# Performance work log

Hardware: AMD Instinct MI355X
Metric: run time of the kernel (lower is better)

Reference implementation:

```python
import jax, jax.numpy as jnp
import numpy as np

B, H, W, DM = 4, 64, 64, 96
DS, DC, K = 16, 3, 4
DI = DM            # expand = 1.0
DTR = 6            # ceil(96/16)


def setup_inputs() -> dict:
    key = jax.random.key(0)
    ks = jax.random.split(key, 12)
    s = 0.02
    # dt bias init exactly as MS2D.dt_init: dt ~ exp(U*(log(max)-log(min))+log(min)); inv softplus
    dt = jnp.exp(jax.random.uniform(ks[5], (K, DI)) * (np.log(0.1) - np.log(0.001)) + np.log(0.001))
    dt = jnp.clip(dt, 1e-4, None)
    inv_dt = dt + jnp.log(-jnp.expm1(-dt))
    A_logs = jnp.log(jnp.broadcast_to(jnp.arange(1, DS + 1, dtype=jnp.float32), (K, DI, DS)))
    return {
        "x": jax.random.normal(ks[0], (B, H, W, DM), jnp.float32),
        "in_proj_w": jax.random.normal(ks[1], (2 * DI, DM), jnp.float32) * s,
        "conv_w": jax.random.normal(ks[2], (DI, 1, DC, DC), jnp.float32) * s,
        "conv_b": jnp.zeros((DI,), jnp.float32),
        "x_proj_weight": jax.random.normal(ks[3], (K, DTR + 2 * DS, DI), jnp.float32) * s,
        "dt_projs_weight": jax.random.uniform(ks[4], (K, DI, DTR), minval=-1.0, maxval=1.0) * (DTR ** -0.5),
        "dt_projs_bias": inv_dt,
        "A_logs": A_logs,
        "Ds": jnp.ones((K, DI), jnp.float32),
        "out_norm_w": jnp.ones((DI,), jnp.float32),
        "out_norm_b": jnp.zeros((DI,), jnp.float32),
        "out_proj_w": jax.random.normal(ks[6], (DM, DI), jnp.float32) * s,
    }


def _ms2d(x, in_proj_w, conv_w, conv_b, x_proj_weight, dt_projs_weight,
          dt_projs_bias, A_logs, Ds, out_norm_w, out_norm_b, out_proj_w):
    Bb, Hh, Ww, _ = x.shape
    L = Hh * Ww
    # in_proj -> (x, z) gating split
    xz = x @ in_proj_w.T                      # (B,H,W,2*DI)
    xc, z = jnp.split(xz, 2, axis=-1)
    xc = jnp.transpose(xc, (0, 3, 1, 2))      # (B,DI,H,W)
    xc = jax.lax.conv_general_dilated(
        xc, conv_w, (1, 1), 'SAME', feature_group_count=xc.shape[1],
        dimension_numbers=('NCHW', 'OIHW', 'NCHW')) + conv_b[None, :, None, None]
    xc = jax.nn.silu(xc)
    d = xc.shape[1]
    # 4-directional scan sequences: hw, wh, and their reverses
    x_hw = xc.reshape(Bb, d, L)
    x_wh = jnp.transpose(xc, (0, 1, 3, 2)).reshape(Bb, d, L)
    x2 = jnp.stack([x_hw, x_wh], axis=1)          # (B,2,d,L)
    xs = jnp.concatenate([x2, jnp.flip(x2, axis=-1)], axis=1)  # (B,4,d,L)
    x_dbl = jnp.einsum('bkdl,kcd->bkcl', xs, x_proj_weight)
    dtr = dt_projs_weight.shape[2]
    n = A_logs.shape[2]
    dts, Bs, Cs = jnp.split(x_dbl, [dtr, dtr + n], axis=2)     # (B,4,r,L),(B,4,N,L),(B,4,N,L)
    dts = jnp.einsum('bkrl,kdr->bkdl', dts, dt_projs_weight)
    delta = jax.nn.softplus(dts + dt_projs_bias[None, :, :, None])  # (B,4,d,L)
    A = -jnp.exp(A_logs)                                        # (4,d,N)
    # time-major for scan
    u_t = jnp.moveaxis(xs, -1, 0)       # (L,B,4,d)
    dl_t = jnp.moveaxis(delta, -1, 0)
    B_t = jnp.moveaxis(Bs, -1, 0)       # (L,B,4,N)
    C_t = jnp.moveaxis(Cs, -1, 0)

    def step(h, inp):                   # h: (B,4,d,N)
        u, dl, b, c = inp
        dA = jnp.exp(dl[..., None] * A)
        h = h * dA + (dl * u)[..., None] * b[:, :, None, :]
        y = jnp.einsum('bkdn,bkn->bkd', h, c)
        return h, y

    h0 = jnp.zeros((Bb, 4, d, n), xs.dtype)
    _, ys = jax.lax.scan(step, h0, (u_t, dl_t, B_t, C_t))
    ys = jnp.moveaxis(ys, 0, -1)        # (B,4,d,L)
    ys = ys + Ds[None, :, :, None] * xs  # skip D*u
    inv_y = jnp.flip(ys[:, 2:4], axis=-1)

    def wh2hw(t):  # undo the (W,H) raster order
        return jnp.transpose(t.reshape(Bb, d, Ww, Hh), (0, 1, 3, 2)).reshape(Bb, d, L)

    y = ys[:, 0] + inv_y[:, 0] + wh2hw(ys[:, 1]) + wh2hw(inv_y[:, 1])
    y = jnp.transpose(y, (0, 2, 1)).reshape(Bb, Hh, Ww, d)
    mu = y.mean(-1, keepdims=True)
    var = y.var(-1, keepdims=True)
    y = (y - mu) / jnp.sqrt(var + 1e-5) * out_norm_w + out_norm_b
    y = y * jax.nn.silu(z)
    return y @ out_proj_w.T


def reference(x, in_proj_w, conv_w, conv_b, x_proj_weight, dt_projs_weight,
              dt_projs_bias, A_logs, Ds, out_norm_w, out_norm_b, out_proj_w):
    return _ms2d(x, in_proj_w, conv_w, conv_b, x_proj_weight, dt_projs_weight,
                 dt_projs_bias, A_logs, Ds, out_norm_w, out_norm_b, out_proj_w)
```

## Files before the change

### kernel.cpp

```cpp
#include <hip/hip_runtime.h>
#include <math.h>


#define LQ 4096
#define NCH 128
#define LCH 32

__device__ __forceinline__ float sigmoid_f(float x){ return 1.0f/(1.0f + __expf(-x)); }
__device__ __forceinline__ float silu_f(float x){ return x * sigmoid_f(x); }
__device__ __forceinline__ float softplus_f(float x){ return (x > 20.0f) ? x : __logf(1.0f + __expf(x)); }

__device__ __forceinline__ int pos_of(int k, int i){
  switch(k & 3){
    case 0: return i;
    case 1: return ((i & 63) << 6) | (i >> 6);
    case 2: return LQ - 1 - i;
    default: { int j = LQ - 1 - i; return ((j & 63) << 6) | (j >> 6); }
  }
}

__device__ __forceinline__ void pow8(float r, int nh, float* e){
  e[0]=r; e[1]=r*r; e[2]=e[1]*r; e[3]=e[1]*e[1];
  e[4]=e[3]*r; e[5]=e[3]*e[1]; e[6]=e[3]*e[2]; e[7]=e[3]*e[3];
  float m = nh ? e[7] : 1.0f;
  #pragma unroll
  for (int j=0;j<8;j++) e[j] *= m;
}

__global__ __launch_bounds__(64) void k_prep(const float* __restrict__ Alogs,
                                             float* __restrict__ An_tab,
                                             float* __restrict__ fflag){
  const int t = blockIdx.x*64 + threadIdx.x;
  if (t >= 384) return;
  bool fast = true;
  #pragma unroll
  for (int n=0;n<16;n++){
    float An = -__expf(Alogs[t*16+n]);
    An_tab[t*16+n] = An;
    fast = fast && (fabsf(An + (float)(n+1)) < 1e-3f*(float)(n+1));
  }
  fflag[t] = fast ? 1.0f : 0.0f;
}

__global__ __launch_bounds__(256) void k_inproj(const float* __restrict__ x,
                                                const float* __restrict__ wproj,
                                                float* __restrict__ xc,
                                                float* __restrict__ zb){
  __shared__ float a_s[64*97];
  __shared__ float w_s[96*97];
  const int t = threadIdx.x;
  const int row0 = (blockIdx.x >> 1) * 64;
  const int ch = blockIdx.x & 1;
  for (int e = t*4; e < 64*96; e += 1024){
    float4 v = *(const float4*)(x + (size_t)row0*96 + e);
    int r = e/96, c = e%96;
    float* p = a_s + r*97 + c;
    p[0]=v.x; p[1]=v.y; p[2]=v.z; p[3]=v.w;
  }
  for (int e = t*4; e < 96*96; e += 1024){
    float4 v = *(const float4*)(wproj + (size_t)ch*96*96 + e);
    int r = e/96, c = e%96;
    float* p = w_s + r*97 + c;
    p[0]=v.x; p[1]=v.y; p[2]=v.z; p[3]=v.w;
  }
  __syncthreads();
  const int tr = t >> 5, tc = t & 31;
  float acc[8][3];
  #pragma unroll
  for (int i=0;i<8;i++){
    #pragma unroll
    for (int j=0;j<3;j++) acc[i][j]=0.f;
  }
  for (int kk=0; kk<96; kk++){
    float a[8], b[3];
    #pragma unroll
    for (int i=0;i<8;i++) a[i] = a_s[(tr*8+i)*97+kk];
    #pragma unroll
    for (int j=0;j<3;j++) b[j] = w_s[(tc*3+j)*97+kk];
    #pragma unroll
    for (int i=0;i<8;i++){
      #pragma unroll
      for (int j=0;j<3;j++) acc[i][j] += a[i]*b[j];
    }
  }
  float* dst = ch ? zb : xc;
  #pragma unroll
  for (int i=0;i<8;i++){
    int row = row0 + tr*8 + i;
    #pragma unroll
    for (int j=0;j<3;j++) dst[(size_t)row*96 + tc*3 + j] = acc[i][j];
  }
}

__global__ __launch_bounds__(256) void k_conv(const float* __restrict__ xc,
                                              const float* __restrict__ cw,
                                              const float* __restrict__ cb,
                                              float* __restrict__ u){
  int e = blockIdx.x*256 + threadIdx.x;
  int d0 = (e % 24) * 4;
  int p = e / 24;
  int w = p & 63, h = (p >> 6) & 63, b = p >> 12;
  float cwv[4][9];
  #pragma unroll
  for (int q=0;q<4;q++){
    #pragma unroll
    for (int tp=0;tp<9;tp++) cwv[q][tp] = cw[(d0+q)*9+tp];
  }
  float4 acc = make_float4(cb[d0], cb[d0+1], cb[d0+2], cb[d0+3]);
  #pragma unroll
  for (int kh=0; kh<3; kh++){
    int hh = h + kh - 1;
    if (hh < 0 || hh > 63) continue;
    #pragma unroll
    for (int kw=0; kw<3; kw++){
      int ww = w + kw - 1;
      if (ww < 0 || ww > 63) continue;
      float4 v = *(const float4*)(xc + ((size_t)((b<<12) + (hh<<6) + ww))*96 + d0);
      int tp = kh*3+kw;
      acc.x += v.x*cwv[0][tp]; acc.y += v.y*cwv[1][tp];
      acc.z += v.z*cwv[2][tp]; acc.w += v.w*cwv[3][tp];
    }
  }
  float4 o = make_float4(silu_f(acc.x), silu_f(acc.y), silu_f(acc.z), silu_f(acc.w));
  *(float4*)(u + (size_t)p*96 + d0) = o;
}

__global__ __launch_bounds__(128) void k_proj(const float* __restrict__ u,
                                              const float* __restrict__ xpw,
                                              float* __restrict__ dts,
                                              float* __restrict__ Bsb,
                                              float* __restrict__ Csb){
  __shared__ float u_s[64*97];
  __shared__ float w_s[40*97];
  const int t = threadIdx.x;
  const int blk = blockIdx.x;
  const int pt = blk & 63, k = (blk >> 6) & 3, b = blk >> 8;
  const int bk = b*4 + k;
  const int i0 = pt * 64;
  for (int e = t*4; e < 64*96; e += 512){
    int row = e/96, c = e%96;
    int p = pos_of(k, i0 + row);
    float4 v = *(const float4*)(u + ((size_t)((b<<12) + p))*96 + c);
    float* dst = u_s + row*97 + c;
    dst[0]=v.x; dst[1]=v.y; dst[2]=v.z; dst[3]=v.w;
  }
  for (int e = t*4; e < 40*96; e += 512){
    int r = e/96, c = e%96;
    float4 v = (r < 38) ? *(const float4*)(xpw + (k*38+r)*96 + c)
                        : make_float4(0,0,0,0);
    float* p = w_s + r*97 + c;
    p[0]=v.x; p[1]=v.y; p[2]=v.z; p[3]=v.w;
  }
  __syncthreads();
  const int posg = t & 15, cg = t >> 4;
  float acc[4][5];
  #pragma unroll
  for (int i=0;i<4;i++){
    #pragma unroll
    for (int j=0;j<5;j++) acc[i][j]=0.f;
  }
  for (int dd=0; dd<96; dd++){
    float uu[4], wv[5];
    #pragma unroll
    for (int i=0;i<4;i++) uu[i] = u_s[(posg*4+i)*97+dd];
    #pragma unroll
    for (int j=0;j<5;j++) wv[j] = w_s[(cg*5+j)*97+dd];
    #pragma unroll
    for (int i=0;i<4;i++){
      #pragma unroll
      for (int j=0;j<5;j++) acc[i][j] += uu[i]*wv[j];
    }
  }
  #pragma unroll
  for (int i=0;i<4;i++){
    int ii = i0 + posg*4 + i;
    int base = (bk<<12) + ii;
    #pragma unroll
    for (int j=0;j<5;j++){
      int c = cg*5 + j;
      float v = acc[i][j];
      if (c < 6)       dts[(size_t)base*6 + c] = v;
      else if (c < 22) Bsb[(size_t)base*16 + (c-6)] = v;
      else if (c < 38) Csb[(size_t)base*16 + (c-22)] = v;
    }
  }
}

__global__ __launch_bounds__(384, 2) void k_scanA2(const float* __restrict__ u,
                                                const float* __restrict__ dts,
                                                const float* __restrict__ Bsb,
                                                const float* __restrict__ Csb,
                                                const float* __restrict__ dtw_g,
                                                const float* __restrict__ dtb_g,
                                                const float* __restrict__ An_tab,
                                                const float* __restrict__ fflag,
                                                float* __restrict__ S,
                                                float* __restrict__ sumd,
                                                float* __restrict__ ys,
                                                float* __restrict__ cum_g){
  const int t = threadIdx.x;
  const int c2 = t / 192;
  const int lane = t & 63;
  const int wv3 = (t % 192) >> 6;
  const int nh = (lane >> 5) & 1;
  const int d = wv3*32 + (lane & 31);
  const int blk = blockIdx.x;
  const int bk = blk >> 6;
  const int k = bk & 3, b = bk >> 2;
  const int chunk = ((blk & 63) << 1) | c2;
  const int ibase = chunk * LCH;
  const int kd = k*96 + d;
  int wfast = __all(fflag[kd] > 0.5f ? 1 : 0);
  float An[8];
  #pragma unroll
  for (int j=0;j<8;j++) An[j] = An_tab[kd*16 + nh*8 + j];
  float dtw[6];
  #pragma unroll
  for (int r=0;r<6;r++) dtw[r] = dtw_g[kd*6+r];
  const float bias = dtb_g[kd];
  const int pb = pos_of(k, ibase);
  const int pstep = pos_of(k, ibase+1) - pb;
  const float* uptr = u + ((size_t)((b<<12)+pb))*96 + d;
  const long ustep = (long)pstep*96;
  const float2* dtp = (const float2*)(dts + ((size_t)((bk<<12)+ibase))*6);
  const float4* Bp = (const float4*)(Bsb + ((size_t)((bk<<12)+ibase))*16) + nh*2;
  const float4* Cp = (const float4*)(Csb + ((size_t)((bk<<12)+ibase))*16) + nh*2;
  float* yp = ys + ((size_t)((bk<<12)+ibase))*96 + d;
  float* cp = cum_g + ((size_t)((bk<<12)+ibase))*96 + d;
  float h[8];
  #pragma unroll
  for (int n=0;n<8;n++) h[n]=0.f;
  float cum = 0.f;
  float u_n = uptr[0];
  float2 q0n = dtp[0], q1n = dtp[1], q2n = dtp[2];
  float4 B0n = Bp[0], B1n = Bp[1];
  float4 C0n = Cp[0], C1n = Cp[1];
  if (wfast){
    #pragma unroll 4
    for (int il=0; il<LCH; il++){
      float u_c = u_n;
      float2 q0=q0n, q1=q1n, q2=q2n;
      float4 B0=B0n, B1=B1n, C0=C0n, C1=C1n;
      const int nx = (il+1 < LCH) ? il+1 : il;
      u_n = uptr[(long)nx*ustep];
      q0n = dtp[nx*3+0]; q1n = dtp[nx*3+1]; q2n = dtp[nx*3+2];
      B0n = Bp[nx*4+0]; B1n = Bp[nx*4+1];
      C0n = Cp[nx*4+0]; C1n = Cp[nx*4+1];
      float accd = bias + dtw[0]*q0.x + dtw[1]*q0.y + dtw[2]*q1.x
                        + dtw[3]*q1.y + dtw[4]*q2.x + dtw[5]*q2.y;
      float t1 = __expf(accd);
      float r = 1.0f/(1.0f+t1);
      float delta = (accd > 20.f) ? accd : __logf(1.0f + t1);
      cum += delta;
      float du = delta * u_c;
      float Bv[8] = {B0.x,B0.y,B0.z,B0.w, B1.x,B1.y,B1.z,B1.w};
      float Cv[8] = {C0.x,C0.y,C0.z,C0.w, C1.x,C1.y,C1.z,C1.w};
      float e[8];
      pow8(r, nh, e);
      float y8 = 0.f;
      #pragma unroll
      for (int n=0;n<8;n++){
        h[n] = h[n]*e[n] + du*Bv[n];
        y8 += h[n]*Cv[n];
      }
      float y = y8 + __shfl_xor(y8, 32, 64);
      if (nh == 0){ yp[(size_t)il*96] = y; cp[(size_t)il*96] = cum; }
    }
  } else {
    #pragma unroll 2
    for (int il=0; il<LCH; il++){
      float u_c = u_n;
      float2 q0=q0n, q1=q1n, q2=q2n;
      float4 B0=B0n, B1=B1n, C0=C0n, C1=C1n;
      const int nx = (il+1 < LCH) ? il+1 : il;
      u_n = uptr[(long)nx*ustep];
      q0n = dtp[nx*3+0]; q1n = dtp[nx*3+1]; q2n = dtp[nx*3+2];
      B0n = Bp[nx*4+0]; B1n = Bp[nx*4+1];
      C0n = Cp[nx*4+0]; C1n = Cp[nx*4+1];
      float accd = bias + dtw[0]*q0.x + dtw[1]*q0.y + dtw[2]*q1.x
                        + dtw[3]*q1.y + dtw[4]*q2.x + dtw[5]*q2.y;
      float delta = softplus_f(accd);
      cum += delta;
      float du = delta * u_c;
      float Bv[8] = {B0.x,B0.y,B0.z,B0.w, B1.x,B1.y,B1.z,B1.w};
      float Cv[8] = {C0.x,C0.y,C0.z,C0.w, C1.x,C1.y,C1.z,C1.w};
      float e[8];
      #pragma unroll
      for (int n=0;n<8;n++) e[n] = __expf(delta*An[n]);
      float y8 = 0.f;
      #pragma unroll
      for (int n=0;n<8;n++){
        h[n] = h[n]*e[n] + du*Bv[n];
        y8 += h[n]*Cv[n];
      }
      float y = y8 + __shfl_xor(y8, 32, 64);
      if (nh == 0){ yp[(size_t)il*96] = y; cp[(size_t)il*96] = cum; }
    }
  }
  const int sb = (bk*NCH + chunk)*96 + d;
  float4* Sp = (float4*)(S + (size_t)sb*16 + nh*8);
  Sp[0] = make_float4(h[0],h[1],h[2],h[3]);
  Sp[1] = make_float4(h[4],h[5],h[6],h[7]);
  if (nh == 0) sumd[sb] = cum;
}

__global__ __launch_bounds__(384) void k_scanA_fb(const float* __restrict__ u,
                                                  const float* __restrict__ dts,
                                                  const float* __restrict__ Bsb,
                                                  const float* __restrict__ dtw_g,
                                                  const float* __restrict__ dtb_g,
                                                  const float* __restrict__ Alogs,
                                                  float* __restrict__ S,
                                                  float* __restrict__ sumd){
  const int t = threadIdx.x;
  const int c2 = t / 192;
  const int lane = t & 63;
  const int wv3 = (t % 192) >> 6;
  const int nh = (lane >> 5) & 1;
  const int d = wv3*32 + (lane & 31);
  const int blk = blockIdx.x;
  const int bk = blk >> 6;
  const int k = bk & 3, b = bk >> 2;
  const int chunk = ((blk & 63) << 1) | c2;
  const int ibase = chunk * LCH;
  float An[8];
  bool fast = true;
  #pragma unroll
  for (int j=0;j<8;j++){
    int n = nh*8 + j;
    An[j] = -__expf(Alogs[(k*96+d)*16+n]);
    fast = fast && (fabsf(An[j] + (float)(n+1)) < 1e-3f*(float)(n+1));
  }
  int wfast = __all(fast ? 1 : 0);
  float dtw[6];
  #pragma unroll
  for (int r=0;r<6;r++) dtw[r] = dtw_g[(k*96+d)*6+r];
  const float bias = dtb_g[k*96+d];
  int pb = pos_of(k, ibase);
  int pstep = pos_of(k, ibase+1) - pb;
  const float* uptr = u + ((size_t)((b<<12)+pb))*96 + d;
  const long ustep = (long)pstep*96;
  const float2* dtp = (const float2*)(dts + ((size_t)((bk<<12)+ibase))*6);
  const float4* Bp = (const float4*)(Bsb + ((size_t)((bk<<12)+ibase))*16) + nh*2;
  float h[8];
  #pragma unroll
  for (int n=0;n<8;n++) h[n]=0.f;
  float sdelta = 0.f;
  #pragma unroll 4
  for (int il=0; il<LCH; il++){
    float uv = *uptr;
    float2 q0 = dtp[0], q1 = dtp[1], q2 = dtp[2];
    float accd = bias + dtw[0]*q0.x + dtw[1]*q0.y + dtw[2]*q1.x
                      + dtw[3]*q1.y + dtw[4]*q2.x + dtw[5]*q2.y;
    float t1 = __expf(accd);
    float r = 1.0f / (1.0f + t1);
    float delta = (accd > 20.f) ? accd : __logf(1.0f + t1);
    sdelta += delta;
    float du = delta * uv;
    float4 b0 = Bp[0], b1 = Bp[1];
    float Bv[8] = {b0.x,b0.y,b0.z,b0.w, b1.x,b1.y,b1.z,b1.w};
    float e[8];
    if (wfast){ pow8(r, nh, e); }
    else {
      #pragma unroll
      for (int n=0;n<8;n++) e[n] = __expf(delta*An[n]);
    }
    #pragma unroll
    for (int n=0;n<8;n++) h[n] = h[n]*e[n] + du*Bv[n];
    uptr += ustep; dtp += 3; Bp += 4;
  }
  const int sb = (bk*NCH + chunk)*96 + d;
  float4* Sp = (float4*)(S + (size_t)sb*16 + nh*8);
  Sp[0] = make_float4(h[0],h[1],h[2],h[3]);
  Sp[1] = make_float4(h[4],h[5],h[6],h[7]);
  if (nh == 0) sumd[sb] = sdelta;
}

__global__ __launch_bounds__(128) void k_scanB2(float* __restrict__ S,
                                                const float* __restrict__ sumd,
                                                const float* __restrict__ Alogs,
                                                const float* __restrict__ An_tab,
                                                const float* __restrict__ fflag){
  __shared__ float As[128*17];
  __shared__ float Bs[128*17];
  const int c = threadIdx.x;
  const int blk = blockIdx.x;
  const int d = blk % 96;
  const int bk = blk / 96;
  const int k = bk & 3;
  const int sb = (bk*NCH + c)*96 + d;
  float a[16], bvals[16];
  {
    const float4* Sp = (const float4*)(S + (size_t)sb*16);
    float4 s0=Sp[0], s1=Sp[1], s2=Sp[2], s3=Sp[3];
    bvals[0]=s0.x;bvals[1]=s0.y;bvals[2]=s0.z;bvals[3]=s0.w;
    bvals[4]=s1.x;bvals[5]=s1.y;bvals[6]=s1.z;bvals[7]=s1.w;
    bvals[8]=s2.x;bvals[9]=s2.y;bvals[10]=s2.z;bvals[11]=s2.w;
    bvals[12]=s3.x;bvals[13]=s3.y;bvals[14]=s3.z;bvals[15]=s3.w;
  }
  const float sd = sumd[sb];
  bool fast;
  float An[16];
  if (An_tab){
    fast = fflag[k*96+d] > 0.5f;
    if (!fast){
      #pragma unroll
      for (int n=0;n<16;n++) An[n] = An_tab[(k*96+d)*16+n];
    }
  } else {
    fast = true;
    #pragma unroll
    for (int n=0;n<16;n++){
      An[n] = -__expf(Alogs[(k*96+d)*16+n]);
      fast = fast && (fabsf(An[n] + (float)(n+1)) < 1e-3f*(float)(n+1));
    }
  }
  if (fast){
    float q = __expf(-sd);
    float p = q;
    #pragma unroll
    for (int n=0;n<16;n++){ a[n] = p; p *= q; }
  } else {
    #pragma unroll
    for (int n=0;n<16;n++) a[n] = __expf(An[n]*sd);
  }
  #pragma unroll
  for (int n=0;n<16;n++){ As[c*17+n] = a[n]; Bs[c*17+n] = bvals[n]; }
  for (int dist=1; dist<128; dist<<=1){
    __syncthreads();
    float aL[16], bL[16];
    if (c >= dist){
      #pragma unroll
      for (int n=0;n<16;n++){ aL[n] = As[(c-dist)*17+n]; bL[n] = Bs[(c-dist)*17+n]; }
    }
    __syncthreads();
    if (c >= dist){
      #pragma unroll
      for (int n=0;n<16;n++){
        bvals[n] = bL[n]*a[n] + bvals[n];
        a[n] = aL[n]*a[n];
        As[c*17+n] = a[n]; Bs[c*17+n] = bvals[n];
      }
    }
  }
  __syncthreads();
  float h0[16];
  #pragma unroll
  for (int n=0;n<16;n++) h0[n] = (c == 0) ? 0.f : Bs[(c-1)*17+n];
  float4* Sp = (float4*)(S + (size_t)sb*16);
  Sp[0] = make_float4(h0[0],h0[1],h0[2],h0[3]);
  Sp[1] = make_float4(h0[4],h0[5],h0[6],h0[7]);
  Sp[2] = make_float4(h0[8],h0[9],h0[10],h0[11]);
  Sp[3] = make_float4(h0[12],h0[13],h0[14],h0[15]);
}

__global__ __launch_bounds__(256) void k_scanY(const float* __restrict__ cum_g,
                                               const float* __restrict__ Csb,
                                               const float* __restrict__ An_tab,
                                               const float* __restrict__ fflag,
                                               const float* __restrict__ h0buf,
                                               float* __restrict__ ys){
  __shared__ float h0_s[32*17];
  __shared__ float An_s[32*17];
  __shared__ float ff_s[32];
  const int t = threadIdx.x;
  const int blk = blockIdx.x;
  const int dslice = blk % 3;
  const int tmp = blk / 3;
  const int chunk = tmp & 127;
  const int bk = tmp >> 7;
  const int k = bk & 3;
  const int dbase = dslice * 32;
  {
    const float* h0src = h0buf + ((size_t)((bk*NCH + chunk)*96 + dbase))*16;
    const float* Ansrc = An_tab + (size_t)(k*96 + dbase)*16;
    for (int e = t; e < 512; e += 256){
      int dl = e >> 4, n = e & 15;
      h0_s[dl*17+n] = h0src[e];
      An_s[dl*17+n] = Ansrc[e];
    }
    if (t < 32) ff_s[t] = fflag[k*96 + dbase + t];
  }
  __syncthreads();
  const int il = t >> 3;
  const int dq = t & 7;
  const int d0 = dbase + dq*4;
  const int i = chunk*LCH + il;
  const size_t rowb = (size_t)((bk<<12) + i);
  float4 cd = *(const float4*)(cum_g + rowb*96 + d0);
  float4 yl = *(const float4*)(ys + rowb*96 + d0);
  float Cv[16];
  {
    const float4* Cp = (const float4*)(Csb + rowb*16);
    float4 c0=Cp[0], c1=Cp[1], c2=Cp[2], c3=Cp[3];
    Cv[0]=c0.x;Cv[1]=c0.y;Cv[2]=c0.z;Cv[3]=c0.w;
    Cv[4]=c1.x;Cv[5]=c1.y;Cv[6]=c1.z;Cv[7]=c1.w;
    Cv[8]=c2.x;Cv[9]=c2.y;Cv[10]=c2.z;Cv[11]=c2.w;
    Cv[12]=c3.x;Cv[13]=c3.y;Cv[14]=c3.z;Cv[15]=c3.w;
  }
  float yout[4] = {yl.x, yl.y, yl.z, yl.w};
  float cdv[4] = {cd.x, cd.y, cd.z, cd.w};
  #pragma unroll
  for (int dd=0; dd<4; dd++){
    const int dl = dq*4 + dd;
    float acc = 0.f;
    if (ff_s[dl] > 0.5f){
      float q = __expf(-cdv[dd]);
      float p = q;
      #pragma unroll
      for (int n=0;n<16;n++){ acc += Cv[n]*h0_s[dl*17+n]*p; p *= q; }
    } else {
      #pragma unroll
      for (int n=0;n<16;n++) acc += Cv[n]*h0_s[dl*17+n]*__expf(An_s[dl*17+n]*cdv[dd]);
    }
    yout[dd] += acc;
  }
  *(float4*)(ys + rowb*96 + d0) = make_float4(yout[0], yout[1], yout[2], yout[3]);
}

__global__ __launch_bounds__(384) void k_scanC_fb(const float* __restrict__ u,
                                                  const float* __restrict__ dts,
                                                  const float* __restrict__ Bsb,
                                                  const float* __restrict__ Csb,
                                                  const float* __restrict__ dtw_g,
                                                  const float* __restrict__ dtb_g,
                                                  const float* __restrict__ Alogs,
                                                  const float* __restrict__ h0buf,
                                                  float* __restrict__ ys){
  const int t = threadIdx.x;
  const int c2 = t / 192;
  const int lane = t & 63;
  const int wv3 = (t % 192) >> 6;
  const int nh = (lane >> 5) & 1;
  const int d = wv3*32 + (lane & 31);
  const int blk = blockIdx.x;
  const int bk = blk >> 6;
  const int k = bk & 3, b = bk >> 2;
  const int chunk = ((blk & 63) << 1) | c2;
  const int ibase = chunk * LCH;
  float An[8];
  bool fast = true;
  #pragma unroll
  for (int j=0;j<8;j++){
    int n = nh*8 + j;
    An[j] = -__expf(Alogs[(k*96+d)*16+n]);
    fast = fast && (fabsf(An[j] + (float)(n+1)) < 1e-3f*(float)(n+1));
  }
  int wfast = __all(fast ? 1 : 0);
  float dtw[6];
  #pragma unroll
  for (int r=0;r<6;r++) dtw[r] = dtw_g[(k*96+d)*6+r];
  const float bias = dtb_g[k*96+d];
  int pb = pos_of(k, ibase);
  int pstep = pos_of(k, ibase+1) - pb;
  const float* uptr = u + ((size_t)((b<<12)+pb))*96 + d;
  const long ustep = (long)pstep*96;
  const float2* dtp = (const float2*)(dts + ((size_t)((bk<<12)+ibase))*6);
  const float4* Bp = (const float4*)(Bsb + ((size_t)((bk<<12)+ibase))*16) + nh*2;
  const float4* Cp = (const float4*)(Csb + ((size_t)((bk<<12)+ibase))*16) + nh*2;
  float* yp = ys + ((size_t)((bk<<12)+ibase))*96 + d;
  float h[8];
  const int sb = (bk*NCH + chunk)*96 + d;
  const float4* Hp = (const float4*)(h0buf + (size_t)sb*16 + nh*8);
  {
    float4 h0=Hp[0], h1=Hp[1];
    h[0]=h0.x;h[1]=h0.y;h[2]=h0.z;h[3]=h0.w;
    h[4]=h1.x;h[5]=h1.y;h[6]=h1.z;h[7]=h1.w;
  }
  #pragma unroll 4
  for (int il=0; il<LCH; il++){
    float uv = *uptr;
    float2 q0 = dtp[0], q1 = dtp[1], q2 = dtp[2];
    float accd = bias + dtw[0]*q0.x + dtw[1]*q0.y + dtw[2]*q1.x
                      + dtw[3]*q1.y + dtw[4]*q2.x + dtw[5]*q2.y;
    float t1 = __expf(accd);
    float r = 1.0f / (1.0f + t1);
    float delta = (accd > 20.f) ? accd : __logf(1.0f + t1);
    float du = delta * uv;
    float4 b0 = Bp[0], b1 = Bp[1];
    float4 c0 = Cp[0], c1 = Cp[1];
    float Bv[8] = {b0.x,b0.y,b0.z,b0.w, b1.x,b1.y,b1.z,b1.w};
    float Cv[8] = {c0.x,c0.y,c0.z,c0.w, c1.x,c1.y,c1.z,c1.w};
    float e[8];
    if (wfast){ pow8(r, nh, e); }
    else {
      #pragma unroll
      for (int n=0;n<8;n++) e[n] = __expf(delta*An[n]);
    }
    float y8 = 0.f;
    #pragma unroll
    for (int n=0;n<8;n++){
      h[n] = h[n]*e[n] + du*Bv[n];
      y8 += h[n]*Cv[n];
    }
    float y = y8 + __shfl_xor(y8, 32, 64);
    if (nh == 0) yp[(size_t)il*96] = y;
    uptr += ustep; dtp += 3; Bp += 4; Cp += 4;
  }
}

__global__ __launch_bounds__(256) void k_out(const float* __restrict__ ys,
                                             const float* __restrict__ ubuf,
                                             const float* __restrict__ Dsg,
                                             const float* __restrict__ zbuf,
                                             const float* __restrict__ nw,
                                             const float* __restrict__ nb,
                                             const float* __restrict__ wout,
                                             float* __restrict__ out){
  __shared__ float w_s[96*97];
  __shared__ float g_s[32*97];
  const int t = threadIdx.x;
  const int b = blockIdx.x >> 7;
  const int pt = blockIdx.x & 127;
  const int p0 = pt * 32;
  for (int e=t*4; e<96*96; e+=1024){
    float4 v = *(const float4*)(wout+e);
    int r=e/96, c=e%96;
    float* p = w_s + r*97 + c;
    p[0]=v.x; p[1]=v.y; p[2]=v.z; p[3]=v.w;
  }
  const int pos = t >> 3, lane8 = t & 7, d0 = lane8*12;
  const int p = p0 + pos;
  const int tp = ((p & 63) << 6) | (p >> 6);
  int idx[4];
  idx[0] = p; idx[1] = tp; idx[2] = LQ-1-p; idx[3] = LQ-1-tp;
  float yv[12];
  float s1=0.f, s2=0.f;
  #pragma unroll
  for (int i=0;i<12;i+=4){
    float4 a = make_float4(0,0,0,0);
    #pragma unroll
    for (int kk=0;kk<4;kk++){
      float4 v = *(const float4*)(ys + ((size_t)(((b*4+kk)<<12) + idx[kk]))*96 + d0 + i);
      a.x+=v.x; a.y+=v.y; a.z+=v.z; a.w+=v.w;
    }
    float4 uv = *(const float4*)(ubuf + ((size_t)((b<<12)+p))*96 + d0 + i);
    #pragma unroll
    for (int q=0;q<4;q++){
      int dd = d0+i+q;
      float sD = Dsg[dd] + Dsg[96+dd] + Dsg[192+dd] + Dsg[288+dd];
      float uq = (q==0)?uv.x:(q==1)?uv.y:(q==2)?uv.z:uv.w;
      float* aq = (q==0)?&a.x:(q==1)?&a.y:(q==2)?&a.z:&a.w;
      *aq += sD * uq;
    }
    yv[i]=a.x; yv[i+1]=a.y; yv[i+2]=a.z; yv[i+3]=a.w;
    s1 += a.x+a.y+a.z+a.w;
    s2 += a.x*a.x + a.y*a.y + a.z*a.z + a.w*a.w;
  }
  #pragma unroll
  for (int m=1; m<8; m<<=1){
    s1 += __shfl_xor(s1, m, 64);
    s2 += __shfl_xor(s2, m, 64);
  }
  const float mu = s1 * (1.0f/96.0f);
  const float var = s2 * (1.0f/96.0f) - mu*mu;
  const float rstd = rsqrtf(var + 1e-5f);
  #pragma unroll
  for (int i=0;i<12;i+=4){
    float4 zv = *(const float4*)(zbuf + ((size_t)((b<<12)+p))*96 + d0 + i);
    float zz[4] = {zv.x,zv.y,zv.z,zv.w};
    #pragma unroll
    for (int q=0;q<4;q++){
      int d = d0+i+q;
      float yn = (yv[i+q]-mu)*rstd*nw[d] + nb[d];
      g_s[pos*97 + d] = yn * silu_f(zz[q]);
    }
  }
  __syncthreads();
  const int posg = t >> 5, mg = t & 31;
  float acc[4][3];
  #pragma unroll
  for (int i=0;i<4;i++){
    #pragma unroll
    for (int j=0;j<3;j++) acc[i][j]=0.f;
  }
  for (int dd=0; dd<96; dd++){
    float g4[4], w3[3];
    #pragma unroll
    for (int i=0;i<4;i++) g4[i] = g_s[(posg*4+i)*97+dd];
    #pragma unroll
    for (int j=0;j<3;j++) w3[j] = w_s[(mg*3+j)*97+dd];
    #pragma unroll
    for (int i=0;i<4;i++){
      #pragma unroll
      for (int j=0;j<3;j++) acc[i][j] += g4[i]*w3[j];
    }
  }
  #pragma unroll
  for (int i=0;i<4;i++){
    int prow = p0 + posg*4 + i;
    #pragma unroll
    for (int j=0;j<3;j++){
      out[((size_t)((b<<12)+prow))*96 + mg*3 + j] = acc[i][j];
    }
  }
}

extern "C" void kernel_launch(void* const* d_in, const int* in_sizes, int n_in,
                              void* d_out, int out_size, void* d_ws, size_t ws_size,
                              hipStream_t stream) {
  (void)in_sizes; (void)n_in; (void)out_size;
  const float* x   = (const float*)d_in[0];
  const float* ipw = (const float*)d_in[1];
  const float* cw  = (const float*)d_in[2];
  const float* cb  = (const float*)d_in[3];
  const float* xpw = (const float*)d_in[4];
  const float* dtw = (const float*)d_in[5];
  const float* dtb = (const float*)d_in[6];
  const float* alg = (const float*)d_in[7];
  const float* dsg = (const float*)d_in[8];
  const float* nw  = (const float*)d_in[9];
  const float* nb  = (const float*)d_in[10];
  const float* wo  = (const float*)d_in[11];
  float* out = (float*)d_out;

  float* w = (float*)d_ws;
  size_t off = 0;
  float* z_b    = w + off; off += 1572864;
  float* u_b    = w + off; off += 1572864;
  float* dts_b  = w + off; off += 393216;
  float* Bs_b   = w + off; off += 1048576;
  float* Cs_b   = w + off; off += 1048576;
  float* Sh_b   = w + off; off += 3145728;
  float* ys_b   = w + off; off += 6291456;
  float* xc_b   = ys_b;
  size_t need_primary = (off + 196608 + 6291456 + 6144 + 384) * sizeof(float);
  float* sumd_ded = w + off;
  float* cum_b    = sumd_ded + 196608;
  float* antab_b  = cum_b + 6291456;
  float* fflag_b  = antab_b + 6144;
  bool primary = (ws_size >= need_primary);
  float* sumd_b = primary ? sumd_ded : ys_b;

  if (primary) k_prep<<<6, 64, 0, stream>>>(alg, antab_b, fflag_b);
  k_inproj<<<512, 256, 0, stream>>>(x, ipw, xc_b, z_b);
  k_conv  <<<1536, 256, 0, stream>>>(xc_b, cw, cb, u_b);
  k_proj  <<<1024, 128, 0, stream>>>(u_b, xpw, dts_b, Bs_b, Cs_b);
  if (primary){
    k_scanA2<<<1024, 384, 0, stream>>>(u_b, dts_b, Bs_b, Cs_b, dtw, dtb,
                                       antab_b, fflag_b, Sh_b, sumd_b, ys_b, cum_b);
    k_scanB2<<<1536, 128, 0, stream>>>(Sh_b, sumd_b, alg, antab_b, fflag_b);
    k_scanY <<<6144, 256, 0, stream>>>(cum_b, Cs_b, antab_b, fflag_b, Sh_b, ys_b);
  } else {
    k_scanA_fb<<<1024, 384, 0, stream>>>(u_b, dts_b, Bs_b, dtw, dtb, alg, Sh_b, sumd_b);
    k_scanB2<<<1536, 128, 0, stream>>>(Sh_b, sumd_b, alg, nullptr, nullptr);
    k_scanC_fb<<<1024, 384, 0, stream>>>(u_b, dts_b, Bs_b, Cs_b, dtw, dtb, alg, Sh_b, ys_b);
  }
  k_out   <<<512, 256, 0, stream>>>(ys_b, u_b, dsg, z_b, nw, nb, wo, out);
}
```

Measured before the change: 230.6 us.

## Precompute softplus decay and delta*u in projection kernel, feed scan via buffers

The dt projection, softplus, decay ratio r and delta*u are now computed in k_proj and written as per-(b,k,position,channel) arrays into the cum and ys buffers. k_scanA2 reads r and du directly, recovers delta as -log(r), and overwrites those buffers in place with cum and y. This takes the dt math and the strided u gather off the latency-critical sequential scan loop. In exchange it adds a full write and re-read of two large arrays, and recovering delta through a log adds rounding error.

```diff
diff --git a/kernel.cpp b/kernel.cpp
--- a/kernel.cpp
+++ b/kernel.cpp
@@ -127,11 +127,16 @@
 
 __global__ __launch_bounds__(128) void k_proj(const float* __restrict__ u,
                                               const float* __restrict__ xpw,
+                                              const float* __restrict__ dtw_g,
+                                              const float* __restrict__ dtb_g,
                                               float* __restrict__ dts,
                                               float* __restrict__ Bsb,
-                                              float* __restrict__ Csb){
+                                              float* __restrict__ Csb,
+                                              float* __restrict__ rg,
+                                              float* __restrict__ dug){
   __shared__ float u_s[64*97];
   __shared__ float w_s[40*97];
+  __shared__ float dtr_s[64*8];
   const int t = threadIdx.x;
   const int blk = blockIdx.x;
   const int pt = blk & 63, k = (blk >> 6) & 3, b = blk >> 8;
@@ -179,25 +184,50 @@
     for (int j=0;j<5;j++){
       int c = cg*5 + j;
       float v = acc[i][j];
-      if (c < 6)       dts[(size_t)base*6 + c] = v;
+      if (c < 6){
+        dts[(size_t)base*6 + c] = v;
+        dtr_s[(posg*4+i)*8 + c] = v;
+      }
       else if (c < 22) Bsb[(size_t)base*16 + (c-6)] = v;
       else if (c < 38) Csb[(size_t)base*16 + (c-22)] = v;
     }
   }
-}
-
-__global__ __launch_bounds__(384, 2) void k_scanA2(const float* __restrict__ u,
-                                                const float* __restrict__ dts,
+  if (rg){
+    __syncthreads();
+    const int pos2 = t >> 1;
+    const int half = t & 1;
+    const int db = half*48;
+    float dtr[6];
+    #pragma unroll
+    for (int r2=0;r2<6;r2++) dtr[r2] = dtr_s[pos2*8+r2];
+    const size_t row = ((size_t)((bk<<12) + i0 + pos2))*96;
+    for (int dd=0; dd<48; dd+=4){
+      float rr[4], dv[4];
+      #pragma unroll
+      for (int q=0;q<4;q++){
+        int d = db+dd+q;
+        const float* wv = dtw_g + (size_t)(k*96+d)*6;
+        float accd = dtb_g[k*96+d] + wv[0]*dtr[0]+wv[1]*dtr[1]+wv[2]*dtr[2]
+                   + wv[3]*dtr[3]+wv[4]*dtr[4]+wv[5]*dtr[5];
+        float t1 = __expf(accd);
+        float delta = (accd > 20.f) ? accd : __logf(1.0f + t1);
+        rr[q] = 1.0f/(1.0f + t1);
+        dv[q] = delta * u_s[pos2*97 + d];
+      }
+      *(float4*)(rg  + row + db+dd) = make_float4(rr[0],rr[1],rr[2],rr[3]);
+      *(float4*)(dug + row + db+dd) = make_float4(dv[0],dv[1],dv[2],dv[3]);
+    }
+  }
+}
+
+__global__ __launch_bounds__(384, 2) void k_scanA2(float* __restrict__ rc,
                                                 const float* __restrict__ Bsb,
                                                 const float* __restrict__ Csb,
-                                                const float* __restrict__ dtw_g,
-                                                const float* __restrict__ dtb_g,
                                                 const float* __restrict__ An_tab,
                                                 const float* __restrict__ fflag,
                                                 float* __restrict__ S,
                                                 float* __restrict__ sumd,
-                                                float* __restrict__ ys,
-                                                float* __restrict__ cum_g){
+                                                float* __restrict__ dy){
   const int t = threadIdx.x;
   const int c2 = t / 192;
   const int lane = t & 63;
@@ -206,82 +236,63 @@
   const int d = wv3*32 + (lane & 31);
   const int blk = blockIdx.x;
   const int bk = blk >> 6;
-  const int k = bk & 3, b = bk >> 2;
+  const int k = bk & 3;
   const int chunk = ((blk & 63) << 1) | c2;
   const int ibase = chunk * LCH;
   const int kd = k*96 + d;
   int wfast = __all(fflag[kd] > 0.5f ? 1 : 0);
-  float An[8];
-  #pragma unroll
-  for (int j=0;j<8;j++) An[j] = An_tab[kd*16 + nh*8 + j];
-  float dtw[6];
-  #pragma unroll
-  for (int r=0;r<6;r++) dtw[r] = dtw_g[kd*6+r];
-  const float bias = dtb_g[kd];
-  const int pb = pos_of(k, ibase);
-  const int pstep = pos_of(k, ibase+1) - pb;
-  const float* uptr = u + ((size_t)((b<<12)+pb))*96 + d;
-  const long ustep = (long)pstep*96;
-  const float2* dtp = (const float2*)(dts + ((size_t)((bk<<12)+ibase))*6);
+  float* rp = rc + ((size_t)((bk<<12)+ibase))*96 + d;
+  float* dp = dy + ((size_t)((bk<<12)+ibase))*96 + d;
   const float4* Bp = (const float4*)(Bsb + ((size_t)((bk<<12)+ibase))*16) + nh*2;
   const float4* Cp = (const float4*)(Csb + ((size_t)((bk<<12)+ibase))*16) + nh*2;
-  float* yp = ys + ((size_t)((bk<<12)+ibase))*96 + d;
-  float* cp = cum_g + ((size_t)((bk<<12)+ibase))*96 + d;
   float h[8];
   #pragma unroll
   for (int n=0;n<8;n++) h[n]=0.f;
   float cum = 0.f;
-  float u_n = uptr[0];
-  float2 q0n = dtp[0], q1n = dtp[1], q2n = dtp[2];
+  float r_n = rp[0];
+  float du_n = dp[0];
   float4 B0n = Bp[0], B1n = Bp[1];
   float4 C0n = Cp[0], C1n = Cp[1];
   if (wfast){
     #pragma unroll 4
     for (int il=0; il<LCH; il++){
-      float u_c = u_n;
-      float2 q0=q0n, q1=q1n, q2=q2n;
+      float r_c = r_n, du_c = du_n;
       float4 B0=B0n, B1=B1n, C0=C0n, C1=C1n;
       const int nx = (il+1 < LCH) ? il+1 : il;
-      u_n = uptr[(long)nx*ustep];
-      q0n = dtp[nx*3+0]; q1n = dtp[nx*3+1]; q2n = dtp[nx*3+2];
+      r_n = rp[(size_t)nx*96];
+      du_n = dp[(size_t)nx*96];
       B0n = Bp[nx*4+0]; B1n = Bp[nx*4+1];
       C0n = Cp[nx*4+0]; C1n = Cp[nx*4+1];
-      float accd = bias + dtw[0]*q0.x + dtw[1]*q0.y + dtw[2]*q1.x
-                        + dtw[3]*q1.y + dtw[4]*q2.x + dtw[5]*q2.y;
-      float t1 = __expf(accd);
-      float r = 1.0f/(1.0f+t1);
-      float delta = (accd > 20.f) ? accd : __logf(1.0f + t1);
+      float delta = -__logf(fmaxf(r_c, 1e-38f));
       cum += delta;
-      float du = delta * u_c;
       float Bv[8] = {B0.x,B0.y,B0.z,B0.w, B1.x,B1.y,B1.z,B1.w};
       float Cv[8] = {C0.x,C0.y,C0.z,C0.w, C1.x,C1.y,C1.z,C1.w};
       float e[8];
-      pow8(r, nh, e);
+      pow8(r_c, nh, e);
       float y8 = 0.f;
       #pragma unroll
       for (int n=0;n<8;n++){
-        h[n] = h[n]*e[n] + du*Bv[n];
+        h[n] = h[n]*e[n] + du_c*Bv[n];
         y8 += h[n]*Cv[n];
       }
       float y = y8 + __shfl_xor(y8, 32, 64);
-      if (nh == 0){ yp[(size_t)il*96] = y; cp[(size_t)il*96] = cum; }
+      if (nh == 0){ dp[(size_t)il*96] = y; rp[(size_t)il*96] = cum; }
     }
   } else {
+    float An[8];
+    #pragma unroll
+    for (int j=0;j<8;j++) An[j] = An_tab[kd*16 + nh*8 + j];
     #pragma unroll 2
     for (int il=0; il<LCH; il++){
-      float u_c = u_n;
-      float2 q0=q0n, q1=q1n, q2=q2n;
+      float r_c = r_n, du_c = du_n;
       float4 B0=B0n, B1=B1n, C0=C0n, C1=C1n;
       const int nx = (il+1 < LCH) ? il+1 : il;
-      u_n = uptr[(long)nx*ustep];
-      q0n = dtp[nx*3+0]; q1n = dtp[nx*3+1]; q2n = dtp[nx*3+2];
+      r_n = rp[(size_t)nx*96];
+      du_n = dp[(size_t)nx*96];
       B0n = Bp[nx*4+0]; B1n = Bp[nx*4+1];
       C0n = Cp[nx*4+0]; C1n = Cp[nx*4+1];
-      float accd = bias + dtw[0]*q0.x + dtw[1]*q0.y + dtw[2]*q1.x
-                        + dtw[3]*q1.y + dtw[4]*q2.x + dtw[5]*q2.y;
-      float delta = softplus_f(accd);
+      float delta = -__logf(fmaxf(r_c, 1e-38f));
       cum += delta;
-      float du = delta * u_c;
       float Bv[8] = {B0.x,B0.y,B0.z,B0.w, B1.x,B1.y,B1.z,B1.w};
       float Cv[8] = {C0.x,C0.y,C0.z,C0.w, C1.x,C1.y,C1.z,C1.w};
       float e[8];
@@ -290,11 +301,11 @@
       float y8 = 0.f;
       #pragma unroll
       for (int n=0;n<8;n++){
-        h[n] = h[n]*e[n] + du*Bv[n];
+        h[n] = h[n]*e[n] + du_c*Bv[n];
         y8 += h[n]*Cv[n];
       }
       float y = y8 + __shfl_xor(y8, 32, 64);
-      if (nh == 0){ yp[(size_t)il*96] = y; cp[(size_t)il*96] = cum; }
+      if (nh == 0){ dp[(size_t)il*96] = y; rp[(size_t)il*96] = cum; }
     }
   }
   const int sb = (bk*NCH + chunk)*96 + d;
@@ -735,10 +746,12 @@
   if (primary) k_prep<<<6, 64, 0, stream>>>(alg, antab_b, fflag_b);
   k_inproj<<<512, 256, 0, stream>>>(x, ipw, xc_b, z_b);
   k_conv  <<<1536, 256, 0, stream>>>(xc_b, cw, cb, u_b);
-  k_proj  <<<1024, 128, 0, stream>>>(u_b, xpw, dts_b, Bs_b, Cs_b);
+  k_proj  <<<1024, 128, 0, stream>>>(u_b, xpw, dtw, dtb, dts_b, Bs_b, Cs_b,
+                                     primary ? cum_b : nullptr,
+                                     primary ? ys_b : nullptr);
   if (primary){
-    k_scanA2<<<1024, 384, 0, stream>>>(u_b, dts_b, Bs_b, Cs_b, dtw, dtb,
-                                       antab_b, fflag_b, Sh_b, sumd_b, ys_b, cum_b);
+    k_scanA2<<<1024, 384, 0, stream>>>(cum_b, Bs_b, Cs_b, antab_b, fflag_b,
+                                       Sh_b, sumd_b, ys_b);
     k_scanB2<<<1536, 128, 0, stream>>>(Sh_b, sumd_b, alg, antab_b, fflag_b);
     k_scanY <<<6144, 256, 0, stream>>>(cum_b, Cs_b, antab_b, fflag_b, Sh_b, ys_b);
   } else {
```

After: 266.0 us. +15.4%, slower.
